# Optimization experiments

Hardware: AMD Instinct MI355X
Metric: run time of the kernel (lower is better)

## Reference

```python
import jax, jax.numpy as jnp
import numpy as np

T, B = 128, 512
NUM_TILES, NUM_COLORS = 16, 16
OBS_EMB, ACT_EMB = 16, 16
NUM_ACTIONS = 6
HIDDEN = 256
ENC_DIM = 5 * 5 * 2 * OBS_EMB + 2 * ACT_EMB + 2  # 834


def setup_inputs() -> dict:
    key = jax.random.key(0)
    ks = jax.random.split(key, 16)
    s = 0.02
    return {
        "obs_img_seq": jax.random.randint(ks[0], (T, B, 5, 5, 2), 0, NUM_TILES, dtype=jnp.int32),
        "obs_dir_seq": jax.random.uniform(ks[1], (T, B, 4), dtype=jnp.float32),
        "prev_action_seq": jax.random.randint(ks[2], (T, B), 0, NUM_ACTIONS, dtype=jnp.int32),
        "prev_reward_seq": jax.random.uniform(ks[3], (T, B), dtype=jnp.float32),
        "done_seq": jnp.zeros((T, B), dtype=jnp.float32),
        "c0": jnp.zeros((B, HIDDEN), dtype=jnp.float32),
        "h0": jnp.zeros((B, HIDDEN), dtype=jnp.float32),
        "tile_emb": jax.random.normal(ks[4], (NUM_TILES, OBS_EMB), jnp.float32) * s,
        "color_emb": jax.random.normal(ks[5], (NUM_COLORS, OBS_EMB), jnp.float32) * s,
        "action_emb": jax.random.normal(ks[6], (NUM_ACTIONS, ACT_EMB), jnp.float32) * s,
        "Wdir": jax.random.normal(ks[7], (4, ACT_EMB), jnp.float32) * s,
        "bdir": jnp.zeros((ACT_EMB,), jnp.float32),
        "W1": jax.random.normal(ks[8], (ENC_DIM, HIDDEN), jnp.float32) * s,
        "b1": jnp.zeros((HIDDEN,), jnp.float32),
        "Wx": jax.random.normal(ks[9], (HIDDEN, 4 * HIDDEN), jnp.float32) * s,
        "Wh": jax.random.normal(ks[10], (HIDDEN, 4 * HIDDEN), jnp.float32) * s,
        "bh": jnp.zeros((4 * HIDDEN,), jnp.float32),
        "Wpi": jax.random.normal(ks[11], (HIDDEN, NUM_ACTIONS), jnp.float32) * s,
        "bpi": jnp.zeros((NUM_ACTIONS,), jnp.float32),
        "Wv": jax.random.normal(ks[12], (HIDDEN, 1), jnp.float32) * s,
        "bv": jnp.zeros((1,), jnp.float32),
    }


def _encode(obs_img, obs_dir, prev_action, prev_reward, done,
            tile_emb, color_emb, action_emb, Wdir, bdir):
    tile = tile_emb[obs_img[..., 0]]          # [T,B,5,5,E]
    color = color_emb[obs_img[..., 1]]        # [T,B,5,5,E]
    img = jnp.concatenate([tile, color], axis=-1)  # [T,B,5,5,2E]
    img_flat = img.reshape(*obs_img.shape[:-3], -1)  # [T,B,50E]
    dir_enc = obs_dir @ Wdir + bdir            # [T,B,ACT_EMB]
    act_enc = action_emb[prev_action]          # [T,B,ACT_EMB]
    return jnp.concatenate(
        [img_flat, dir_enc, act_enc, prev_reward[..., None], done[..., None]], axis=-1)


def reference(obs_img_seq, obs_dir_seq, prev_action_seq, prev_reward_seq, done_seq,
              c0, h0, tile_emb, color_emb, action_emb, Wdir, bdir,
              W1, b1, Wx, Wh, bh, Wpi, bpi, Wv, bv):
    enc = _encode(obs_img_seq, obs_dir_seq, prev_action_seq, prev_reward_seq, done_seq,
                  tile_emb, color_emb, action_emb, Wdir, bdir)  # [T,B,ENC_DIM]
    x = jax.nn.relu(jnp.einsum("tbe,eh->tbh", enc, W1) + b1)     # [T,B,H]
    xg = jnp.einsum("tbh,hg->tbg", x, Wx)                        # [T,B,4H] input gates

    def cell(carry, xg_t):
        c, h = carry
        z = xg_t + h @ Wh + bh
        i, f, g, o = jnp.split(z, 4, axis=-1)
        new_c = jax.nn.sigmoid(f) * c + jax.nn.sigmoid(i) * jnp.tanh(g)
        new_h = jax.nn.sigmoid(o) * jnp.tanh(new_c)
        return (new_c, new_h), new_h

    (cf, hf), h_seq = jax.lax.scan(cell, (c0, h0), xg)           # h_seq: [T,B,H]
    logits = jnp.einsum("tbh,ha->tba", h_seq, Wpi) + bpi         # [T,B,A]
    values = jnp.einsum("tbh,hv->tbv", h_seq, Wv) + bv           # [T,B,1]
    return logits, values, (cf, hf)
```

## Files before the change

### kernel.cpp

```cpp
#include <hip/hip_runtime.h>
#include <hip/hip_bf16.h>


#define WS_TT   0u
#define WS_CT   409600u
#define WS_AT   819200u
#define WS_WD1  825344u
#define WS_B1T  829440u
#define WS_WRW  830464u
#define WS_WDN  831488u
#define WS_W2T  1048576u
#define WS_HDB  2097152u
#define WS_X    4194304u
#define WS_NEED (WS_X + 33554432u)

typedef __attribute__((ext_vector_type(8))) short s8v;
typedef __attribute__((ext_vector_type(4))) float f4v;
typedef __attribute__((ext_vector_type(4))) unsigned u4v;
typedef unsigned short u16;
typedef unsigned char u8;

union U4 { u4v v4; unsigned u[4]; };

__device__ __forceinline__ float sigm_(float x) {
  return __builtin_amdgcn_rcpf(1.f + __expf(-x));
}
__device__ __forceinline__ float tanh_(float x) {
  return 1.f - 2.f * __builtin_amdgcn_rcpf(1.f + __expf(2.f * x));
}

__global__ __launch_bounds__(256) void k_prep(
    const float* tile_emb, const float* color_emb, const float* action_emb,
    const float* Wdir, const float* bdir, const float* W1, const float* b1,
    const float* Wx, const float* Wh, const float* h0, const float* bpi,
    const float* bv, float* out, char* ws) {
  int id = blockIdx.x;
  int h = threadIdx.x;
  if (id < 816) {
    float* TT  = (float*)(ws + WS_TT);
    float* CT  = (float*)(ws + WS_CT);
    float* AT  = (float*)(ws + WS_AT);
    float* WD1 = (float*)(ws + WS_WD1);
    float* B1T = (float*)(ws + WS_B1T);
    float* WRW = (float*)(ws + WS_WRW);
    float* WDN = (float*)(ws + WS_WDN);
    if (id < 400) {
      int p = id >> 4, v = id & 15;
      float s = 0.f;
#pragma unroll
      for (int e = 0; e < 16; ++e) s += tile_emb[v * 16 + e] * W1[(p * 32 + e) * 256 + h];
      TT[id * 256 + h] = s;
    } else if (id < 800) {
      int p = (id - 400) >> 4, v = id & 15;
      float s = 0.f;
#pragma unroll
      for (int e = 0; e < 16; ++e) s += color_emb[v * 16 + e] * W1[(p * 32 + 16 + e) * 256 + h];
      CT[(id - 400) * 256 + h] = s;
    } else {
      int r = id - 800;
      if (r < 6) {
        float s = 0.f;
#pragma unroll
        for (int e = 0; e < 16; ++e) s += action_emb[r * 16 + e] * W1[(816 + e) * 256 + h];
        AT[r * 256 + h] = s;
      } else if (r < 10) {
        int d = r - 6;
        float s = 0.f;
#pragma unroll
        for (int e = 0; e < 16; ++e) s += Wdir[d * 16 + e] * W1[(800 + e) * 256 + h];
        WD1[d * 256 + h] = s;
      } else if (r == 10) {
        float s = b1[h];
#pragma unroll
        for (int e = 0; e < 16; ++e) s += bdir[e] * W1[(800 + e) * 256 + h];
        B1T[h] = s;
      } else if (r == 11) {
        WRW[h] = W1[832 * 256 + h];
      } else if (r == 12) {
        WDN[h] = W1[833 * 256 + h];
      }
    }
  } else if (id < 944) {
    int wb = id - 816;
#pragma unroll
    for (int kk = 0; kk < 4; ++kk) {
      int k = wb * 4 + kk;
      const float* row = (k < 256) ? (Wx + (size_t)k * 1024)
                                   : (Wh + (size_t)(k - 256) * 1024);
      float4 v4 = *(const float4*)(row + h * 4);
      float vv[4] = {v4.x, v4.y, v4.z, v4.w};
#pragma unroll
      for (int e = 0; e < 4; ++e) {
        int n = h * 4 + e;
        int gate = n >> 8, rem = n & 255;
        int q = rem >> 5, jl = rem & 31;
        int pcl = (jl >> 2) * 16 + (jl & 3) * 4 + gate;
        unsigned byteoff = ((unsigned)(pcl << 10) + (unsigned)(k << 1)) ^
                           (((unsigned)(pcl & 7)) << 4);
        __hip_bfloat16 bv16 = __float2bfloat16(vv[e]);
        *(u16*)(ws + WS_W2T + (size_t)q * 131072u + byteoff) = *(u16*)&bv16;
      }
    }
  } else {
    int mb = id - 944;
    int i = mb * 256 + h;
    if (mb < 512) {
      unsigned* hdb = (unsigned*)(ws + WS_HDB);
      __hip_bfloat16 hb = __float2bfloat16(h0[i]);
      hdb[i] = (unsigned)*(u16*)&hb;
    } else if (mb < 2048) {
      int j = i - 131072;
      out[j] = bpi[j % 6];
    } else {
      int j = i - 524288;
      out[393216 + j] = bv[0];
    }
  }
}

__global__ __launch_bounds__(512, 1) void k_x(
    const int* obs_img, const float* obs_dir, const int* prev_action,
    const float* prev_reward, const float* done, char* ws) {
  __shared__ float TtL[12800];
  __shared__ float CtL[12800];
  __shared__ float AtL[192];
  __shared__ float WdL[128];
  __shared__ u8 pkT[6400];
  __shared__ u8 pkC[6400];
  __shared__ u8 actL[256];
  __shared__ float rewL[256];
  __shared__ float dnL[256];
  __shared__ float dirL[1024];

  const float* TT  = (const float*)(ws + WS_TT);
  const float* CT  = (const float*)(ws + WS_CT);
  const float* AT  = (const float*)(ws + WS_AT);
  const float* WD1 = (const float*)(ws + WS_WD1);
  const float* B1T = (const float*)(ws + WS_B1T);
  const float* WRW = (const float*)(ws + WS_WRW);
  const float* WDN = (const float*)(ws + WS_WDN);
  __hip_bfloat16* xout = (__hip_bfloat16*)(ws + WS_X);

  int bid = blockIdx.x;
  int slice = bid & 7, grp = bid >> 3;
  int h0 = slice * 32;
  int tid = threadIdx.x;
  int sub = tid >> 5, hh = tid & 31;

  for (int e = tid; e < 12800; e += 512) {
    int pv = e >> 5, k = e & 31;
    TtL[e] = TT[pv * 256 + h0 + k];
    CtL[e] = CT[pv * 256 + h0 + k];
  }
  for (int e = tid; e < 192; e += 512) AtL[e] = AT[(e >> 5) * 256 + h0 + (e & 31)];
  for (int e = tid; e < 128; e += 512) WdL[e] = WD1[(e >> 5) * 256 + h0 + (e & 31)];
  float b1r = B1T[h0 + hh], wrr = WRW[h0 + hh], wdr = WDN[h0 + hh];

  for (int cg = 0; cg < 4; ++cg) {
    int tb0 = grp * 1024 + cg * 256;
    __syncthreads();
    for (int e = tid; e < 6400; e += 512) {
      int tbl = e / 25, p = e - tbl * 25;
      int base = ((tb0 + tbl) * 25 + p) * 2;
      pkT[e] = (u8)obs_img[base];
      pkC[e] = (u8)obs_img[base + 1];
    }
    for (int e = tid; e < 256; e += 512) {
      actL[e] = (u8)prev_action[tb0 + e];
      rewL[e] = prev_reward[tb0 + e];
      dnL[e]  = done[tb0 + e];
    }
    for (int e = tid; e < 1024; e += 512) dirL[e] = obs_dir[(size_t)tb0 * 4 + e];
    __syncthreads();

    for (int pass = 0; pass < 16; ++pass) {
      int tbl = pass * 16 + sub;
      float s0 = b1r, s1 = 0.f;
#pragma unroll
      for (int p = 0; p < 25; ++p) {
        int tv = pkT[tbl * 25 + p];
        int cv = pkC[tbl * 25 + p];
        s0 += TtL[(p * 16 + tv) * 32 + hh];
        s1 += CtL[(p * 16 + cv) * 32 + hh];
      }
      s0 += AtL[(int)actL[tbl] * 32 + hh];
      float d0 = dirL[tbl * 4 + 0], d1 = dirL[tbl * 4 + 1];
      float d2 = dirL[tbl * 4 + 2], d3 = dirL[tbl * 4 + 3];
      s1 += d0 * WdL[hh] + d1 * WdL[32 + hh] + d2 * WdL[64 + hh] + d3 * WdL[96 + hh];
      s0 += rewL[tbl] * wrr + dnL[tbl] * wdr;
      float xv = fmaxf(s0 + s1, 0.f);
      xout[(size_t)(tb0 + tbl) * 256 + h0 + hh] = __float2bfloat16(xv);
    }
  }
}

__global__ __launch_bounds__(256, 1) void k_lstm(
    const float* c0, const float* bh, const float* Wpi, const float* Wv,
    float* out, char* ws) {
  __shared__ u16 W2T[65536];
  __shared__ float WpiL[32][8];
  __shared__ float part[2][4][16][8];
  __shared__ unsigned hstage[2][16 * 36];

  const u16* xbf = (const u16*)(ws + WS_X);
  unsigned* hdb = (unsigned*)(ws + WS_HDB);
  const u16* w2src = (const u16*)(ws + WS_W2T);

  const int tid = threadIdx.x;
  const int bid = blockIdx.x;
  const int c = bid & 31;
  const int q = bid >> 5;
  const int b0 = c * 16;
  const int lane = tid & 63, wv = tid >> 6;
  const int G = lane >> 4, bl = lane & 15;

  {
    const s8v* src = (const s8v*)(w2src + (size_t)q * 65536);
    s8v* dst = (s8v*)W2T;
    for (int i = tid; i < 8192; i += 256) dst[i] = src[i];
  }
  {
    int jl = tid >> 3, a = tid & 7;
    int j = q * 32 + jl;
    WpiL[jl][a] = (a < 6) ? Wpi[j * 6 + a] : ((a == 6) ? Wv[j] : 0.f);
  }
  __syncthreads();

  const int jt0 = wv * 2, jt1 = wv * 2 + 1;
  const int jl0 = jt0 * 4 + G, jl1 = jt1 * 4 + G;
  const int myhj0 = q * 32 + jl0, myhj1 = q * 32 + jl1;
  const unsigned swz = ((unsigned)(bl & 7)) << 4;
  const unsigned ab0 = ((unsigned)(jt0 * 16 + bl)) << 10;
  const unsigned ab1 = ((unsigned)(jt1 * 16 + bl)) << 10;

  float bh0r[4], bh1r[4];
#pragma unroll
  for (int r = 0; r < 4; ++r) {
    bh0r[r] = bh[r * 256 + myhj0];
    bh1r[r] = bh[r * 256 + myhj1];
  }
  float cst0 = c0[(size_t)(b0 + bl) * 256 + myhj0];
  float cst1 = c0[(size_t)(b0 + bl) * 256 + myhj1];

  float* out_logits = out;
  float* out_values = out + 393216;
  float* out_cf = out + 458752;
  float* out_hf = out + 589824;

  for (int t = 0; t < 128; ++t) {
    s8v xf[8];
    const u16* xr = xbf + ((size_t)t * 512 + (b0 + bl)) * 256 + 8 * G;
#pragma unroll
    for (int ks = 0; ks < 8; ++ks)
      asm volatile("global_load_dwordx4 %0, %1, off"
                   : "=v"(xf[ks]) : "v"(xr + ks * 32));

    U4 qv[16];
    const unsigned* hp = hdb + (size_t)(t & 1) * 131072u +
                         (size_t)(b0 + bl) * 256u + (unsigned)(G * 8);
#pragma unroll
    for (int i = 0; i < 16; ++i) {
      if ((i >> 1) != q || t == 0)
        asm volatile("global_load_dwordx4 %0, %1, off sc0 sc1"
                     : "=v"(qv[i].v4) : "v"(hp + (i >> 1) * 32 + (i & 1) * 4));
    }
    asm volatile("s_waitcnt vmcnt(0)" ::: "memory");
    __builtin_amdgcn_sched_barrier(0);

    const unsigned tq = (unsigned)t;
    bool ok = true;
#pragma unroll
    for (int i = 0; i < 16; ++i) {
      if ((i >> 1) == q && t != 0) continue;
#pragma unroll
      for (int c2 = 0; c2 < 4; ++c2) ok &= ((qv[i].u[c2] >> 16) == tq);
    }
    while (!ok) {
      __builtin_amdgcn_s_sleep(2);
#pragma unroll
      for (int i = 0; i < 16; ++i) {
        if ((i >> 1) != q || t == 0)
          asm volatile("global_load_dwordx4 %0, %1, off sc0 sc1"
                       : "=v"(qv[i].v4) : "v"(hp + (i >> 1) * 32 + (i & 1) * 4));
      }
      asm volatile("s_waitcnt vmcnt(0)" ::: "memory");
      __builtin_amdgcn_sched_barrier(0);
      ok = true;
#pragma unroll
      for (int i = 0; i < 16; ++i) {
        if ((i >> 1) == q && t != 0) continue;
#pragma unroll
        for (int c2 = 0; c2 < 4; ++c2) ok &= ((qv[i].u[c2] >> 16) == tq);
      }
    }

    f4v acc0 = {0.f, 0.f, 0.f, 0.f};
    f4v acc1 = {0.f, 0.f, 0.f, 0.f};
#pragma unroll
    for (int ks = 0; ks < 8; ++ks) {
      unsigned k2 = (unsigned)(ks * 64 + G * 16);
      s8v a0 = *(const s8v*)((const char*)W2T + ((ab0 + k2) ^ swz));
      s8v a1 = *(const s8v*)((const char*)W2T + ((ab1 + k2) ^ swz));
      acc0 = __builtin_amdgcn_mfma_f32_16x16x32_bf16(a0, xf[ks], acc0, 0, 0, 0);
      acc1 = __builtin_amdgcn_mfma_f32_16x16x32_bf16(a1, xf[ks], acc1, 0, 0, 0);
    }
#pragma unroll
    for (int ks = 0; ks < 8; ++ks) {
      union { s8v v; unsigned u[4]; } bu;
      if (ks == q && t != 0) {
        const unsigned* hs = &hstage[t & 1][bl * 36 + G * 8];
        bu.u[0] = (hs[0] & 0xffffu) | (hs[1] << 16);
        bu.u[1] = (hs[2] & 0xffffu) | (hs[3] << 16);
        bu.u[2] = (hs[4] & 0xffffu) | (hs[5] << 16);
        bu.u[3] = (hs[6] & 0xffffu) | (hs[7] << 16);
      } else {
        const unsigned* pa = qv[ks * 2].u;
        const unsigned* pb = qv[ks * 2 + 1].u;
        bu.u[0] = (pa[0] & 0xffffu) | (pa[1] << 16);
        bu.u[1] = (pa[2] & 0xffffu) | (pa[3] << 16);
        bu.u[2] = (pb[0] & 0xffffu) | (pb[1] << 16);
        bu.u[3] = (pb[2] & 0xffffu) | (pb[3] << 16);
      }
      unsigned k2 = (unsigned)((ks + 8) * 64 + G * 16);
      s8v a0 = *(const s8v*)((const char*)W2T + ((ab0 + k2) ^ swz));
      s8v a1 = *(const s8v*)((const char*)W2T + ((ab1 + k2) ^ swz));
      acc0 = __builtin_amdgcn_mfma_f32_16x16x32_bf16(a0, bu.v, acc0, 0, 0, 0);
      acc1 = __builtin_amdgcn_mfma_f32_16x16x32_bf16(a1, bu.v, acc1, 0, 0, 0);
    }

    float zi0 = acc0[0] + bh0r[0], zf0 = acc0[1] + bh0r[1];
    float zg0 = acc0[2] + bh0r[2], zo0 = acc0[3] + bh0r[3];
    float cn0 = sigm_(zf0) * cst0 + sigm_(zi0) * tanh_(zg0);
    float hn0 = sigm_(zo0) * tanh_(cn0);
    cst0 = cn0;
    float zi1 = acc1[0] + bh1r[0], zf1 = acc1[1] + bh1r[1];
    float zg1 = acc1[2] + bh1r[2], zo1 = acc1[3] + bh1r[3];
    float cn1 = sigm_(zf1) * cst1 + sigm_(zi1) * tanh_(zg1);
    float hn1 = sigm_(zo1) * tanh_(cn1);
    cst1 = cn1;

    const int wslot = (t + 1) & 1, pt = t & 1;
    if (t < 127) {
      __hip_bfloat16 hb0 = __float2bfloat16(hn0);
      __hip_bfloat16 hb1 = __float2bfloat16(hn1);
      hstage[wslot][bl * 36 + jl0] = ((unsigned)(t + 1) << 16) | (unsigned)*(u16*)&hb0;
      hstage[wslot][bl * 36 + jl1] = ((unsigned)(t + 1) << 16) | (unsigned)*(u16*)&hb1;
    } else {
      size_t o = (size_t)(b0 + bl) * 256;
      out_cf[o + myhj0] = cst0;
      out_cf[o + myhj1] = cst1;
      out_hf[o + myhj0] = hn0;
      out_hf[o + myhj1] = hn1;
    }
    float pl[7];
#pragma unroll
    for (int a = 0; a < 7; ++a) {
      float s = hn0 * WpiL[jl0][a] + hn1 * WpiL[jl1][a];
      s += __shfl_xor(s, 16, 64);
      s += __shfl_xor(s, 32, 64);
      pl[a] = s;
    }
    if (lane < 16) {
#pragma unroll
      for (int a = 0; a < 7; ++a) part[pt][wv][bl][a] = pl[a];
    }

    __syncthreads();

    if (tid < 128) {
      if (t < 127) {
        int b_ = tid >> 3, quad = tid & 7;
        U4 v;
        v.u[0] = hstage[wslot][b_ * 36 + quad * 4 + 0];
        v.u[1] = hstage[wslot][b_ * 36 + quad * 4 + 1];
        v.u[2] = hstage[wslot][b_ * 36 + quad * 4 + 2];
        v.u[3] = hstage[wslot][b_ * 36 + quad * 4 + 3];
        unsigned* dst = hdb + (size_t)wslot * 131072u +
                        (size_t)(b0 + b_) * 256u + (unsigned)(q * 32 + quad * 4);
        asm volatile("global_store_dwordx4 %0, %1, off sc0 sc1"
                     :: "v"(dst), "v"(v.v4) : "memory");
      }
    } else {
      int i2 = tid - 128, b_ = i2 >> 3, a_ = i2 & 7;
      if (a_ < 7) {
        float s = part[pt][0][b_][a_] + part[pt][1][b_][a_] +
                  part[pt][2][b_][a_] + part[pt][3][b_][a_];
        if (a_ < 6)
          atomicAdd(out_logits + ((size_t)t * 512 + b0 + b_) * 6 + a_, s);
        else
          atomicAdd(out_values + (size_t)t * 512 + b0 + b_, s);
      }
    }
  }
}

extern "C" void kernel_launch(void* const* d_in, const int* in_sizes, int n_in,
                              void* d_out, int out_size, void* d_ws, size_t ws_size,
                              hipStream_t stream) {
  const int*   obs_img     = (const int*)d_in[0];
  const float* obs_dir     = (const float*)d_in[1];
  const int*   prev_action = (const int*)d_in[2];
  const float* prev_reward = (const float*)d_in[3];
  const float* done        = (const float*)d_in[4];
  const float* c0          = (const float*)d_in[5];
  const float* h0          = (const float*)d_in[6];
  const float* tile_emb    = (const float*)d_in[7];
  const float* color_emb   = (const float*)d_in[8];
  const float* action_emb  = (const float*)d_in[9];
  const float* Wdir        = (const float*)d_in[10];
  const float* bdir        = (const float*)d_in[11];
  const float* W1          = (const float*)d_in[12];
  const float* b1          = (const float*)d_in[13];
  const float* Wx          = (const float*)d_in[14];
  const float* Wh          = (const float*)d_in[15];
  const float* bh          = (const float*)d_in[16];
  const float* Wpi         = (const float*)d_in[17];
  const float* bpi         = (const float*)d_in[18];
  const float* Wv          = (const float*)d_in[19];
  const float* bv          = (const float*)d_in[20];
  (void)in_sizes; (void)n_in; (void)out_size; (void)ws_size;

  char* ws = (char*)d_ws;
  float* out = (float*)d_out;

  (void)hipMemsetAsync(ws + WS_HDB, 0xAA, 1048576u, stream);
  k_prep<<<3248, 256, 0, stream>>>(tile_emb, color_emb, action_emb, Wdir, bdir,
                                   W1, b1, Wx, Wh, h0, bpi, bv, out, ws);
  k_x<<<512, 512, 0, stream>>>(obs_img, obs_dir, prev_action, prev_reward, done, ws);
  k_lstm<<<256, 256, 0, stream>>>(c0, bh, Wpi, Wv, out, ws);
}
```

Measured before the change: 1.032 ms.

## Process four batch slices per LSTM block and overlap x-gemm with h loads

Reduces the LSTM grid from 256 to 64 blocks, each now handling four 16-row batch slices sequentially per timestep with per-slice cell state and staging buffers. The input-gate MFMAs are issued while the cross-block hidden-state loads are still in flight (partial vmcnt wait) before spinning on the flag check. This cuts the number of blocks taking part in the global flag-based synchronisation, but serialises four slices per block per step, lengthening the per-step critical path and using fewer CUs.

```diff
diff --git a/kernel.cpp b/kernel.cpp
--- a/kernel.cpp
+++ b/kernel.cpp
@@ -200,7 +200,7 @@
   __shared__ u16 W2T[65536];
   __shared__ float WpiL[32][8];
   __shared__ float part[2][4][16][8];
-  __shared__ unsigned hstage[2][16 * 36];
+  __shared__ unsigned hstage[4][2][576];
 
   const u16* xbf = (const u16*)(ws + WS_X);
   unsigned* hdb = (unsigned*)(ws + WS_HDB);
@@ -208,9 +208,8 @@
 
   const int tid = threadIdx.x;
   const int bid = blockIdx.x;
-  const int c = bid & 31;
-  const int q = bid >> 5;
-  const int b0 = c * 16;
+  const int g = bid & 7;
+  const int q = bid >> 3;
   const int lane = tid & 63, wv = tid >> 6;
   const int G = lane >> 4, bl = lane & 15;
 
@@ -239,8 +238,13 @@
     bh0r[r] = bh[r * 256 + myhj0];
     bh1r[r] = bh[r * 256 + myhj1];
   }
-  float cst0 = c0[(size_t)(b0 + bl) * 256 + myhj0];
-  float cst1 = c0[(size_t)(b0 + bl) * 256 + myhj1];
+  float cs0[4], cs1[4];
+#pragma unroll
+  for (int s = 0; s < 4; ++s) {
+    int b0s = (g * 4 + s) * 16;
+    cs0[s] = c0[(size_t)(b0s + bl) * 256 + myhj0];
+    cs1[s] = c0[(size_t)(b0s + bl) * 256 + myhj1];
+  }
 
   float* out_logits = out;
   float* out_values = out + 393216;
@@ -248,147 +252,156 @@
   float* out_hf = out + 589824;
 
   for (int t = 0; t < 128; ++t) {
-    s8v xf[8];
-    const u16* xr = xbf + ((size_t)t * 512 + (b0 + bl)) * 256 + 8 * G;
-#pragma unroll
-    for (int ks = 0; ks < 8; ++ks)
-      asm volatile("global_load_dwordx4 %0, %1, off"
-                   : "=v"(xf[ks]) : "v"(xr + ks * 32));
-
-    U4 qv[16];
-    const unsigned* hp = hdb + (size_t)(t & 1) * 131072u +
-                         (size_t)(b0 + bl) * 256u + (unsigned)(G * 8);
-#pragma unroll
-    for (int i = 0; i < 16; ++i) {
-      if ((i >> 1) != q || t == 0)
-        asm volatile("global_load_dwordx4 %0, %1, off sc0 sc1"
-                     : "=v"(qv[i].v4) : "v"(hp + (i >> 1) * 32 + (i & 1) * 4));
-    }
-    asm volatile("s_waitcnt vmcnt(0)" ::: "memory");
-    __builtin_amdgcn_sched_barrier(0);
-
     const unsigned tq = (unsigned)t;
-    bool ok = true;
-#pragma unroll
-    for (int i = 0; i < 16; ++i) {
-      if ((i >> 1) == q && t != 0) continue;
-#pragma unroll
-      for (int c2 = 0; c2 < 4; ++c2) ok &= ((qv[i].u[c2] >> 16) == tq);
-    }
-    while (!ok) {
-      __builtin_amdgcn_s_sleep(2);
+#pragma unroll
+    for (int s = 0; s < 4; ++s) {
+      const int b0s = (g * 4 + s) * 16;
+      s8v xf[8];
+      const u16* xr = xbf + ((size_t)t * 512 + (b0s + bl)) * 256 + 8 * G;
+#pragma unroll
+      for (int ks = 0; ks < 8; ++ks)
+        asm volatile("global_load_dwordx4 %0, %1, off"
+                     : "=v"(xf[ks]) : "v"(xr + ks * 32));
+
+      U4 qv[16];
+      const unsigned* hp = hdb + (size_t)(t & 1) * 131072u +
+                           (size_t)(b0s + bl) * 256u + (unsigned)(G * 8);
 #pragma unroll
       for (int i = 0; i < 16; ++i) {
         if ((i >> 1) != q || t == 0)
           asm volatile("global_load_dwordx4 %0, %1, off sc0 sc1"
                        : "=v"(qv[i].v4) : "v"(hp + (i >> 1) * 32 + (i & 1) * 4));
       }
+      asm volatile("s_waitcnt vmcnt(14)" ::: "memory");
+      __builtin_amdgcn_sched_barrier(0);
+
+      f4v acc0 = {0.f, 0.f, 0.f, 0.f};
+      f4v acc1 = {0.f, 0.f, 0.f, 0.f};
+#pragma unroll
+      for (int ks = 0; ks < 8; ++ks) {
+        unsigned k2 = (unsigned)(ks * 64 + G * 16);
+        s8v a0 = *(const s8v*)((const char*)W2T + ((ab0 + k2) ^ swz));
+        s8v a1 = *(const s8v*)((const char*)W2T + ((ab1 + k2) ^ swz));
+        acc0 = __builtin_amdgcn_mfma_f32_16x16x32_bf16(a0, xf[ks], acc0, 0, 0, 0);
+        acc1 = __builtin_amdgcn_mfma_f32_16x16x32_bf16(a1, xf[ks], acc1, 0, 0, 0);
+      }
       asm volatile("s_waitcnt vmcnt(0)" ::: "memory");
       __builtin_amdgcn_sched_barrier(0);
-      ok = true;
+
+      bool ok = true;
 #pragma unroll
       for (int i = 0; i < 16; ++i) {
         if ((i >> 1) == q && t != 0) continue;
 #pragma unroll
         for (int c2 = 0; c2 < 4; ++c2) ok &= ((qv[i].u[c2] >> 16) == tq);
       }
-    }
-
-    f4v acc0 = {0.f, 0.f, 0.f, 0.f};
-    f4v acc1 = {0.f, 0.f, 0.f, 0.f};
-#pragma unroll
-    for (int ks = 0; ks < 8; ++ks) {
-      unsigned k2 = (unsigned)(ks * 64 + G * 16);
-      s8v a0 = *(const s8v*)((const char*)W2T + ((ab0 + k2) ^ swz));
-      s8v a1 = *(const s8v*)((const char*)W2T + ((ab1 + k2) ^ swz));
-      acc0 = __builtin_amdgcn_mfma_f32_16x16x32_bf16(a0, xf[ks], acc0, 0, 0, 0);
-      acc1 = __builtin_amdgcn_mfma_f32_16x16x32_bf16(a1, xf[ks], acc1, 0, 0, 0);
-    }
-#pragma unroll
-    for (int ks = 0; ks < 8; ++ks) {
-      union { s8v v; unsigned u[4]; } bu;
-      if (ks == q && t != 0) {
-        const unsigned* hs = &hstage[t & 1][bl * 36 + G * 8];
-        bu.u[0] = (hs[0] & 0xffffu) | (hs[1] << 16);
-        bu.u[1] = (hs[2] & 0xffffu) | (hs[3] << 16);
-        bu.u[2] = (hs[4] & 0xffffu) | (hs[5] << 16);
-        bu.u[3] = (hs[6] & 0xffffu) | (hs[7] << 16);
+      while (!ok) {
+        __builtin_amdgcn_s_sleep(2);
+#pragma unroll
+        for (int i = 0; i < 16; ++i) {
+          if ((i >> 1) != q || t == 0)
+            asm volatile("global_load_dwordx4 %0, %1, off sc0 sc1"
+                         : "=v"(qv[i].v4) : "v"(hp + (i >> 1) * 32 + (i & 1) * 4));
+        }
+        asm volatile("s_waitcnt vmcnt(0)" ::: "memory");
+        __builtin_amdgcn_sched_barrier(0);
+        ok = true;
+#pragma unroll
+        for (int i = 0; i < 16; ++i) {
+          if ((i >> 1) == q && t != 0) continue;
+#pragma unroll
+          for (int c2 = 0; c2 < 4; ++c2) ok &= ((qv[i].u[c2] >> 16) == tq);
+        }
+      }
+
+#pragma unroll
+      for (int ks = 0; ks < 8; ++ks) {
+        union { s8v v; unsigned u[4]; } bu;
+        if (ks == q && t != 0) {
+          const unsigned* hs = &hstage[s][t & 1][bl * 36 + G * 8];
+          bu.u[0] = (hs[0] & 0xffffu) | (hs[1] << 16);
+          bu.u[1] = (hs[2] & 0xffffu) | (hs[3] << 16);
+          bu.u[2] = (hs[4] & 0xffffu) | (hs[5] << 16);
+          bu.u[3] = (hs[6] & 0xffffu) | (hs[7] << 16);
+        } else {
+          const unsigned* pa = qv[ks * 2].u;
+          const unsigned* pb = qv[ks * 2 + 1].u;
+          bu.u[0] = (pa[0] & 0xffffu) | (pa[1] << 16);
+          bu.u[1] = (pa[2] & 0xffffu) | (pa[3] << 16);
+          bu.u[2] = (pb[0] & 0xffffu) | (pb[1] << 16);
+          bu.u[3] = (pb[2] & 0xffffu) | (pb[3] << 16);
+        }
+        unsigned k2 = (unsigned)((ks + 8) * 64 + G * 16);
+        s8v a0 = *(const s8v*)((const char*)W2T + ((ab0 + k2) ^ swz));
+        s8v a1 = *(const s8v*)((const char*)W2T + ((ab1 + k2) ^ swz));
+        acc0 = __builtin_amdgcn_mfma_f32_16x16x32_bf16(a0, bu.v, acc0, 0, 0, 0);
+        acc1 = __builtin_amdgcn_mfma_f32_16x16x32_bf16(a1, bu.v, acc1, 0, 0, 0);
+      }
+
+      float zi0 = acc0[0] + bh0r[0], zf0 = acc0[1] + bh0r[1];
+      float zg0 = acc0[2] + bh0r[2], zo0 = acc0[3] + bh0r[3];
+      float cn0 = sigm_(zf0) * cs0[s] + sigm_(zi0) * tanh_(zg0);
+      float hn0 = sigm_(zo0) * tanh_(cn0);
+      cs0[s] = cn0;
+      float zi1 = acc1[0] + bh1r[0], zf1 = acc1[1] + bh1r[1];
+      float zg1 = acc1[2] + bh1r[2], zo1 = acc1[3] + bh1r[3];
+      float cn1 = sigm_(zf1) * cs1[s] + sigm_(zi1) * tanh_(zg1);
+      float hn1 = sigm_(zo1) * tanh_(cn1);
+      cs1[s] = cn1;
+
+      const int wslot = (t + 1) & 1, pt = s & 1;
+      if (t < 127) {
+        __hip_bfloat16 hb0 = __float2bfloat16(hn0);
+        __hip_bfloat16 hb1 = __float2bfloat16(hn1);
+        hstage[s][wslot][bl * 36 + jl0] =
+            ((unsigned)(t + 1) << 16) | (unsigned)*(u16*)&hb0;
+        hstage[s][wslot][bl * 36 + jl1] =
+            ((unsigned)(t + 1) << 16) | (unsigned)*(u16*)&hb1;
       } else {
-        const unsigned* pa = qv[ks * 2].u;
-        const unsigned* pb = qv[ks * 2 + 1].u;
-        bu.u[0] = (pa[0] & 0xffffu) | (pa[1] << 16);
-        bu.u[1] = (pa[2] & 0xffffu) | (pa[3] << 16);
-        bu.u[2] = (pb[0] & 0xffffu) | (pb[1] << 16);
-        bu.u[3] = (pb[2] & 0xffffu) | (pb[3] << 16);
-      }
-      unsigned k2 = (unsigned)((ks + 8) * 64 + G * 16);
-      s8v a0 = *(const s8v*)((const char*)W2T + ((ab0 + k2) ^ swz));
-      s8v a1 = *(const s8v*)((const char*)W2T + ((ab1 + k2) ^ swz));
-      acc0 = __builtin_amdgcn_mfma_f32_16x16x32_bf16(a0, bu.v, acc0, 0, 0, 0);
-      acc1 = __builtin_amdgcn_mfma_f32_16x16x32_bf16(a1, bu.v, acc1, 0, 0, 0);
-    }
-
-    float zi0 = acc0[0] + bh0r[0], zf0 = acc0[1] + bh0r[1];
-    float zg0 = acc0[2] + bh0r[2], zo0 = acc0[3] + bh0r[3];
-    float cn0 = sigm_(zf0) * cst0 + sigm_(zi0) * tanh_(zg0);
-    float hn0 = sigm_(zo0) * tanh_(cn0);
-    cst0 = cn0;
-    float zi1 = acc1[0] + bh1r[0], zf1 = acc1[1] + bh1r[1];
-    float zg1 = acc1[2] + bh1r[2], zo1 = acc1[3] + bh1r[3];
-    float cn1 = sigm_(zf1) * cst1 + sigm_(zi1) * tanh_(zg1);
-    float hn1 = sigm_(zo1) * tanh_(cn1);
-    cst1 = cn1;
-
-    const int wslot = (t + 1) & 1, pt = t & 1;
-    if (t < 127) {
-      __hip_bfloat16 hb0 = __float2bfloat16(hn0);
-      __hip_bfloat16 hb1 = __float2bfloat16(hn1);
-      hstage[wslot][bl * 36 + jl0] = ((unsigned)(t + 1) << 16) | (unsigned)*(u16*)&hb0;
-      hstage[wslot][bl * 36 + jl1] = ((unsigned)(t + 1) << 16) | (unsigned)*(u16*)&hb1;
-    } else {
-      size_t o = (size_t)(b0 + bl) * 256;
-      out_cf[o + myhj0] = cst0;
-      out_cf[o + myhj1] = cst1;
-      out_hf[o + myhj0] = hn0;
-      out_hf[o + myhj1] = hn1;
-    }
-    float pl[7];
-#pragma unroll
-    for (int a = 0; a < 7; ++a) {
-      float s = hn0 * WpiL[jl0][a] + hn1 * WpiL[jl1][a];
-      s += __shfl_xor(s, 16, 64);
-      s += __shfl_xor(s, 32, 64);
-      pl[a] = s;
-    }
-    if (lane < 16) {
-#pragma unroll
-      for (int a = 0; a < 7; ++a) part[pt][wv][bl][a] = pl[a];
-    }
-
-    __syncthreads();
-
-    if (tid < 128) {
-      if (t < 127) {
-        int b_ = tid >> 3, quad = tid & 7;
-        U4 v;
-        v.u[0] = hstage[wslot][b_ * 36 + quad * 4 + 0];
-        v.u[1] = hstage[wslot][b_ * 36 + quad * 4 + 1];
-        v.u[2] = hstage[wslot][b_ * 36 + quad * 4 + 2];
-        v.u[3] = hstage[wslot][b_ * 36 + quad * 4 + 3];
-        unsigned* dst = hdb + (size_t)wslot * 131072u +
-                        (size_t)(b0 + b_) * 256u + (unsigned)(q * 32 + quad * 4);
-        asm volatile("global_store_dwordx4 %0, %1, off sc0 sc1"
-                     :: "v"(dst), "v"(v.v4) : "memory");
-      }
-    } else {
-      int i2 = tid - 128, b_ = i2 >> 3, a_ = i2 & 7;
-      if (a_ < 7) {
-        float s = part[pt][0][b_][a_] + part[pt][1][b_][a_] +
-                  part[pt][2][b_][a_] + part[pt][3][b_][a_];
-        if (a_ < 6)
-          atomicAdd(out_logits + ((size_t)t * 512 + b0 + b_) * 6 + a_, s);
-        else
-          atomicAdd(out_values + (size_t)t * 512 + b0 + b_, s);
+        size_t o = (size_t)(b0s + bl) * 256;
+        out_cf[o + myhj0] = cs0[s];
+        out_cf[o + myhj1] = cs1[s];
+        out_hf[o + myhj0] = hn0;
+        out_hf[o + myhj1] = hn1;
+      }
+      float pl[7];
+#pragma unroll
+      for (int a = 0; a < 7; ++a) {
+        float sv = hn0 * WpiL[jl0][a] + hn1 * WpiL[jl1][a];
+        sv += __shfl_xor(sv, 16, 64);
+        sv += __shfl_xor(sv, 32, 64);
+        pl[a] = sv;
+      }
+      if (lane < 16) {
+#pragma unroll
+        for (int a = 0; a < 7; ++a) part[pt][wv][bl][a] = pl[a];
+      }
+
+      __syncthreads();
+
+      if (tid < 128) {
+        if (t < 127) {
+          int b_ = tid >> 3, quad = tid & 7;
+          U4 v;
+          v.u[0] = hstage[s][wslot][b_ * 36 + quad * 4 + 0];
+          v.u[1] = hstage[s][wslot][b_ * 36 + quad * 4 + 1];
+          v.u[2] = hstage[s][wslot][b_ * 36 + quad * 4 + 2];
+          v.u[3] = hstage[s][wslot][b_ * 36 + quad * 4 + 3];
+          unsigned* dst = hdb + (size_t)wslot * 131072u +
+                          (size_t)(b0s + b_) * 256u + (unsigned)(q * 32 + quad * 4);
+          asm volatile("global_store_dwordx4 %0, %1, off sc0 sc1"
+                       :: "v"(dst), "v"(v.v4) : "memory");
+        }
+      } else {
+        int i2 = tid - 128, b_ = i2 >> 3, a_ = i2 & 7;
+        if (a_ < 7) {
+          float sv = part[pt][0][b_][a_] + part[pt][1][b_][a_] +
+                     part[pt][2][b_][a_] + part[pt][3][b_][a_];
+          if (a_ < 6)
+            atomicAdd(out_logits + ((size_t)t * 512 + b0s + b_) * 6 + a_, sv);
+          else
+            atomicAdd(out_values + (size_t)t * 512 + b0s + b_, sv);
+        }
       }
     }
   }
@@ -427,5 +440,5 @@
   k_prep<<<3248, 256, 0, stream>>>(tile_emb, color_emb, action_emb, Wdir, bdir,
                                    W1, b1, Wx, Wh, h0, bpi, bv, out, ws);
   k_x<<<512, 512, 0, stream>>>(obs_img, obs_dir, prev_action, prev_reward, done, ws);
-  k_lstm<<<256, 256, 0, stream>>>(c0, bh, Wpi, Wv, out, ws);
-}
+  k_lstm<<<64, 256, 0, stream>>>(c0, bh, Wpi, Wv, out, ws);
+}
```

New measurement: 2.670 ms. 2.59x slower.
